# Optimization experiments

Measured on AMD Instinct MI355X. Metric: run time of the kernel, lower is better.

Reference implementation:

```python
import jax, jax.numpy as jnp
import numpy as np

N = 100000       # nodes
E = 3200000      # edges
F_IN = 128       # num_node_features
DIM = 32         # hidden dim (fixed in Net1)
L = 3            # num_layers
C = 10           # num_classes


def setup_inputs() -> dict:
    key = jax.random.key(0)
    ks = jax.random.split(key, 16)
    x = jax.random.normal(ks[0], (N, F_IN), dtype=jnp.float32)
    src = jax.random.randint(ks[1], (E,), 0, N, dtype=jnp.int32)
    dst = jax.random.randint(ks[2], (E,), 0, N, dtype=jnp.int32)
    def glorot(k, shape):
        lim = np.sqrt(6.0 / (shape[0] + shape[1])).astype(np.float32)
        return jax.random.uniform(k, shape, jnp.float32, -lim, lim)
    dims = [F_IN, DIM, DIM]
    inp = {"x": x, "src": src, "dst": dst}
    for i in range(L):
        din = dims[i]
        inp[f"Wn{i}"] = glorot(ks[3 + 3 * i], (din, DIM))      # neighbor weight
        inp[f"bn{i}"] = jnp.zeros((DIM,), jnp.float32)          # neighbor bias
        inp[f"Ws{i}"] = glorot(ks[4 + 3 * i], (din, DIM))      # self weight (no bias)
    inp["fc_w"] = glorot(ks[13], (DIM * L + F_IN, C))
    inp["fc_b"] = jnp.zeros((C,), jnp.float32)
    return inp


def _graph_conv_wl(x, src, dst, Wn, bn, Ws):
    # GraphConv(norm='none'): transform then aggregate (sum over in-neighbors)
    h = x @ Wn                                   # [N, DIM]
    msg = h[src]                                 # [E, DIM] gather
    agg = jax.ops.segment_sum(msg, dst, num_segments=N)  # [N, DIM] scatter-add
    return agg + bn + x @ Ws


def reference(x, src, dst, Wn0, bn0, Ws0, Wn1, bn1, Ws1, Wn2, bn2, Ws2, fc_w, fc_b):
    params = [(Wn0, bn0, Ws0), (Wn1, bn1, Ws1), (Wn2, bn2, Ws2)]
    xs = [x]
    h = x
    for Wn, bn, Ws in params:
        h = jax.nn.relu(_graph_conv_wl(h, src, dst, Wn, bn, Ws))
        xs.append(h)
    h = jnp.concatenate(xs, axis=1)              # [N, 128 + 3*32]
    logits = h @ fc_w + fc_b                     # [N, C]
    return jax.nn.log_softmax(logits, axis=1)
```

## Files before the change

kernel.cpp:

```cpp
#include <hip/hip_runtime.h>
#include <cstdint>

#define NN 100000
#define EE 3200000
#define SB_BITS 8
#define SB_NODES (1 << SB_BITS)
#define NSB ((NN + SB_NODES - 1) / SB_NODES)
#define CAP 9216
#define CH 4096
#define EPT (CH / 256)

__device__ inline float4 add4(float4 a, float4 b) {
    return make_float4(a.x + b.x, a.y + b.y, a.z + b.z, a.w + b.w);
}

__device__ inline unsigned pk_bf2(float lo, float hi) {
    unsigned a = __float_as_uint(lo);
    unsigned b = __float_as_uint(hi);
    a = (a + 0x7FFFu + ((a >> 16) & 1u)) >> 16;
    b = (b + 0x7FFFu + ((b >> 16) & 1u)) & 0xFFFF0000u;
    return a | b;
}


__global__ void k_hist_sb(const int* __restrict__ dst, int* __restrict__ scnt) {
    __shared__ int h[NSB];
    for (int i = threadIdx.x; i < NSB; i += 256) h[i] = 0;
    __syncthreads();
    for (int e = blockIdx.x * 256 + threadIdx.x; e < EE; e += gridDim.x * 256)
        atomicAdd(&h[dst[e] >> SB_BITS], 1);
    __syncthreads();
    for (int i = threadIdx.x; i < NSB; i += 256) {
        int v = h[i];
        if (v) atomicAdd(&scnt[i], v);
    }
}

__global__ void k_scan_sb(const int* __restrict__ scnt,
                          int* __restrict__ sbptr, int* __restrict__ cursor) {
    __shared__ int sm[512];
    int i = threadIdx.x;
    int v0 = (i < NSB) ? scnt[i] : 0;
    int v1 = (i + 256 < NSB) ? scnt[i + 256] : 0;
    sm[i] = v0;
    sm[i + 256] = v1;
    __syncthreads();
    for (int o = 1; o < 512; o <<= 1) {
        int a0 = (i >= o) ? sm[i - o] : 0;
        int a1 = (i + 256 >= o) ? sm[i + 256 - o] : 0;
        __syncthreads();
        sm[i] += a0;
        sm[i + 256] += a1;
        __syncthreads();
    }
    if (i < NSB)       { sbptr[i]       = sm[i] - v0;       cursor[i]       = sm[i] - v0; }
    if (i + 256 < NSB) { sbptr[i + 256] = sm[i + 256] - v1; cursor[i + 256] = sm[i + 256] - v1; }
    if (i == 0) sbptr[NSB] = sm[511];
}

__global__ void k_split(const int* __restrict__ src, const int* __restrict__ dst,
                        int* __restrict__ cursor, int* __restrict__ out) {
    __shared__ int hist[512];
    __shared__ int lbase[NSB];
    __shared__ int gbase[NSB];
    __shared__ int buf[CH];
    __shared__ unsigned short keyb[CH];
    const int nchunks = (EE + CH - 1) / CH;
    for (int c = blockIdx.x; c < nchunks; c += gridDim.x) {
        int base = c * CH;
        int cnt = min(CH, EE - base);
        hist[threadIdx.x] = 0;
        hist[threadIdx.x + 256] = 0;
        __syncthreads();
        int words[EPT], ranks[EPT], keys[EPT];
        #pragma unroll
        for (int k = 0; k < EPT; ++k) {
            int idx = threadIdx.x + k * 256;
            if (idx < cnt) {
                int d = dst[base + idx];
                int s = src[base + idx];
                int key = d >> SB_BITS;
                words[k] = s | ((d & (SB_NODES - 1)) << 17);
                keys[k] = key;
                ranks[k] = atomicAdd(&hist[key], 1);
            } else keys[k] = -1;
        }
        __syncthreads();
        int i = threadIdx.x;
        int v0 = hist[i], v1 = hist[i + 256];
        for (int o = 1; o < 512; o <<= 1) {
            int a0 = (i >= o) ? hist[i - o] : 0;
            int a1 = (i + 256 >= o) ? hist[i + 256 - o] : 0;
            __syncthreads();
            hist[i] += a0;
            hist[i + 256] += a1;
            __syncthreads();
        }
        if (i < NSB) {
            lbase[i] = hist[i] - v0;
            gbase[i] = (v0 > 0) ? atomicAdd(&cursor[i], v0) : 0;
        }
        if (i + 256 < NSB) {
            lbase[i + 256] = hist[i + 256] - v1;
            gbase[i + 256] = (v1 > 0) ? atomicAdd(&cursor[i + 256], v1) : 0;
        }
        __syncthreads();
        #pragma unroll
        for (int k = 0; k < EPT; ++k) {
            if (keys[k] >= 0) {
                int p = lbase[keys[k]] + ranks[k];
                buf[p] = words[k];
                keyb[p] = (unsigned short)keys[k];
            }
        }
        __syncthreads();
        for (int j = threadIdx.x; j < cnt; j += 256) {
            int kk = keyb[j];
            out[gbase[kk] + (j - lbase[kk])] = buf[j];
        }
        __syncthreads();
    }
}

__global__ void k_sb_sort(const int* __restrict__ sbptr, const int* __restrict__ packed,
                          int* __restrict__ csr_src, int* __restrict__ rowptr) {
    __shared__ int hist[SB_NODES];
    __shared__ int lbuf[CAP];
    int b = blockIdx.x;
    int e0 = sbptr[b], e1 = sbptr[b + 1];
    int cnt = e1 - e0;
    hist[threadIdx.x] = 0;
    __syncthreads();
    for (int j = e0 + threadIdx.x; j < e1; j += 256)
        atomicAdd(&hist[(packed[j] >> 17) & (SB_NODES - 1)], 1);
    __syncthreads();
    int i = threadIdx.x;
    int v = hist[i];
    for (int o = 1; o < 256; o <<= 1) {
        int a = (i >= o) ? hist[i - o] : 0;
        __syncthreads();
        hist[i] += a;
        __syncthreads();
    }
    int excl = hist[i] - v;
    int node = (b << SB_BITS) + i;
    if (node < NN) rowptr[node] = e0 + excl;
    hist[i] = excl;
    if (b == 0 && i == 0) rowptr[NN] = EE;
    __syncthreads();
    if (cnt <= CAP) {
        for (int j = e0 + threadIdx.x; j < e1; j += 256) {
            int w = packed[j];
            int n = (w >> 17) & (SB_NODES - 1);
            int pos = atomicAdd(&hist[n], 1);
            lbuf[pos] = w & 0x1FFFF;
        }
        __syncthreads();
        for (int j = threadIdx.x; j < cnt; j += 256)
            csr_src[e0 + j] = lbuf[j];
    } else {
        for (int j = e0 + threadIdx.x; j < e1; j += 256) {
            int w = packed[j];
            int n = (w >> 17) & (SB_NODES - 1);
            int pos = atomicAdd(&hist[n], 1);
            csr_src[e0 + pos] = w & 0x1FFFF;
        }
    }
}


template <int DIN>
__global__ __launch_bounds__(256) void k_transform(
        const float* __restrict__ h,
        const float* __restrict__ Wn,
        const float* __restrict__ Ws,
        const float* __restrict__ bn,
        unsigned* __restrict__ t_bf,
        float* __restrict__ hout) {
    constexpr int KC = 16;
    __shared__ float hs[256 * (KC + 1)];
    const int which = blockIdx.x & 1;
    const int node = (blockIdx.x >> 1) * 256 + threadIdx.x;
    const bool valid = node < NN;
    const float* __restrict__ W = which ? Ws : Wn;
    const float* __restrict__ hr = h + (size_t)(valid ? node : NN - 1) * DIN;
    float acc[32];
    #pragma unroll
    for (int d = 0; d < 32; ++d) acc[d] = 0.f;
    for (int kc = 0; kc < DIN; kc += KC) {
        __syncthreads();
        #pragma unroll
        for (int j = 0; j < KC / 4; ++j) {
            float4 f = *(const float4*)(hr + kc + j * 4);
            hs[threadIdx.x * (KC + 1) + j * 4 + 0] = f.x;
            hs[threadIdx.x * (KC + 1) + j * 4 + 1] = f.y;
            hs[threadIdx.x * (KC + 1) + j * 4 + 2] = f.z;
            hs[threadIdx.x * (KC + 1) + j * 4 + 3] = f.w;
        }
        __syncthreads();
        #pragma unroll
        for (int kk = 0; kk < KC; ++kk) {
            float f = hs[threadIdx.x * (KC + 1) + kk];
            const float* __restrict__ w0 = W + (kc + kk) * 32;
            #pragma unroll
            for (int d = 0; d < 32; ++d) acc[d] = fmaf(f, w0[d], acc[d]);
        }
    }
    if (valid) {
        if (which) {
            float* __restrict__ hp = hout + (size_t)node * 32;
            #pragma unroll
            for (int d = 0; d < 32; d += 4)
                *(float4*)(hp + d) = make_float4(acc[d] + bn[d], acc[d + 1] + bn[d + 1],
                                                 acc[d + 2] + bn[d + 2], acc[d + 3] + bn[d + 3]);
        } else {
            unsigned tb[16];
            #pragma unroll
            for (int d = 0; d < 16; ++d) tb[d] = pk_bf2(acc[2 * d], acc[2 * d + 1]);
            unsigned* tp = t_bf + (size_t)node * 16;
            #pragma unroll
            for (int d = 0; d < 16; d += 4)
                *(uint4*)(tp + d) = make_uint4(tb[d], tb[d + 1], tb[d + 2], tb[d + 3]);
        }
    }
}

__global__ void k_aggregate(const int* __restrict__ rowptr,
                            const int* __restrict__ csr_src,
                            const uint2* __restrict__ t2,
                            float4* __restrict__ hout4) {
    int node = blockIdx.x * 32 + (threadIdx.x >> 3);
    int q = threadIdx.x & 7;
    if (node >= NN) return;
    int j = rowptr[node];
    int end = rowptr[node + 1];
    float4 a0 = make_float4(0.f, 0.f, 0.f, 0.f);
    float4 a1 = a0, a2 = a0, a3 = a0;
    for (; j + 4 <= end; j += 4) {
        int s0 = csr_src[j];
        int s1 = csr_src[j + 1];
        int s2 = csr_src[j + 2];
        int s3 = csr_src[j + 3];
        uint2 u0 = t2[s0 * 8 + q];
        uint2 u1 = t2[s1 * 8 + q];
        uint2 u2 = t2[s2 * 8 + q];
        uint2 u3 = t2[s3 * 8 + q];
        a0.x += __uint_as_float(u0.x << 16); a0.y += __uint_as_float(u0.x & 0xFFFF0000u);
        a0.z += __uint_as_float(u0.y << 16); a0.w += __uint_as_float(u0.y & 0xFFFF0000u);
        a1.x += __uint_as_float(u1.x << 16); a1.y += __uint_as_float(u1.x & 0xFFFF0000u);
        a1.z += __uint_as_float(u1.y << 16); a1.w += __uint_as_float(u1.y & 0xFFFF0000u);
        a2.x += __uint_as_float(u2.x << 16); a2.y += __uint_as_float(u2.x & 0xFFFF0000u);
        a2.z += __uint_as_float(u2.y << 16); a2.w += __uint_as_float(u2.y & 0xFFFF0000u);
        a3.x += __uint_as_float(u3.x << 16); a3.y += __uint_as_float(u3.x & 0xFFFF0000u);
        a3.z += __uint_as_float(u3.y << 16); a3.w += __uint_as_float(u3.y & 0xFFFF0000u);
    }
    for (; j < end; ++j) {
        uint2 u = t2[csr_src[j] * 8 + q];
        a0.x += __uint_as_float(u.x << 16); a0.y += __uint_as_float(u.x & 0xFFFF0000u);
        a0.z += __uint_as_float(u.y << 16); a0.w += __uint_as_float(u.y & 0xFFFF0000u);
    }
    float4 s = add4(add4(a0, a1), add4(a2, a3));
    int idx = node * 8 + q;
    float4 h = hout4[idx];
    h.x = fmaxf(h.x + s.x, 0.f);
    h.y = fmaxf(h.y + s.y, 0.f);
    h.z = fmaxf(h.z + s.z, 0.f);
    h.w = fmaxf(h.w + s.w, 0.f);
    hout4[idx] = h;
}

__global__ void k_final(const float* __restrict__ x,
                        const float* __restrict__ h1,
                        const float* __restrict__ h2,
                        const float* __restrict__ h3,
                        const float* __restrict__ fc_w,
                        const float* __restrict__ fc_b,
                        float* __restrict__ out) {
    __shared__ float Wl[224 * 10];
    __shared__ float bl[10];
    for (int i = threadIdx.x; i < 224 * 10; i += blockDim.x) Wl[i] = fc_w[i];
    if (threadIdx.x < 10) bl[threadIdx.x] = fc_b[threadIdx.x];
    __syncthreads();
    int n = blockIdx.x * blockDim.x + threadIdx.x;
    if (n >= NN) return;
    float acc[10];
    #pragma unroll
    for (int c = 0; c < 10; ++c) acc[c] = bl[c];
    const float* xr = x + (size_t)n * 128;
    for (int j = 0; j < 128; ++j) {
        float f = xr[j];
        #pragma unroll
        for (int c = 0; c < 10; ++c) acc[c] += f * Wl[j * 10 + c];
    }
    const float* hs[3] = {h1, h2, h3};
    for (int l = 0; l < 3; ++l) {
        const float* hr = hs[l] + (size_t)n * 32;
        for (int j = 0; j < 32; ++j) {
            float f = hr[j];
            #pragma unroll
            for (int c = 0; c < 10; ++c) acc[c] += f * Wl[(128 + l * 32 + j) * 10 + c];
        }
    }
    float m = acc[0];
    #pragma unroll
    for (int c = 1; c < 10; ++c) m = fmaxf(m, acc[c]);
    float s = 0.f;
    #pragma unroll
    for (int c = 0; c < 10; ++c) s += __expf(acc[c] - m);
    float ls = __logf(s);
    #pragma unroll
    for (int c = 0; c < 10; ++c) out[n * 10 + c] = acc[c] - m - ls;
}

extern "C" void kernel_launch(void* const* d_in, const int* in_sizes, int n_in,
                              void* d_out, int out_size, void* d_ws, size_t ws_size,
                              hipStream_t stream) {
    const float* x   = (const float*)d_in[0];
    const int*   src = (const int*)d_in[1];
    const int*   dst = (const int*)d_in[2];
    const float* Wn[3] = {(const float*)d_in[3], (const float*)d_in[6], (const float*)d_in[9]};
    const float* bn[3] = {(const float*)d_in[4], (const float*)d_in[7], (const float*)d_in[10]};
    const float* Ws[3] = {(const float*)d_in[5], (const float*)d_in[8], (const float*)d_in[11]};
    const float* fc_w = (const float*)d_in[12];
    const float* fc_b = (const float*)d_in[13];
    float* out = (float*)d_out;

    char* w = (char*)d_ws;
    const size_t NF = (size_t)NN * 32;
    unsigned* t_bf = (unsigned*)w;              w += (size_t)NN * 16 * 4;
    float* h1  = (float*)w;                     w += NF * 4;
    float* h2  = (float*)w;                     w += NF * 4;
    float* h3  = (float*)w;                     w += NF * 4;
    int* csr_src = (int*)w;                     w += (size_t)EE * 4;
    int* scnt   = (int*)w;                      w += (size_t)NSB * 4;
    int* sbptr  = (int*)w;                      w += (size_t)(NSB + 1) * 4;
    int* cursor = (int*)w;                      w += (size_t)NSB * 4;
    int* rowptr = (int*)w;                      w += (size_t)(NN + 1) * 4;
    int* packed = (int*)h3;

    hipMemsetAsync(scnt, 0, (size_t)NSB * 4, stream);
    k_hist_sb<<<512, 256, 0, stream>>>(dst, scnt);
    k_scan_sb<<<1, 256, 0, stream>>>(scnt, sbptr, cursor);
    k_split<<<512, 256, 0, stream>>>(src, dst, cursor, packed);
    k_sb_sort<<<NSB, 256, 0, stream>>>(sbptr, packed, csr_src, rowptr);

    const int tr_blocks = 2 * ((NN + 255) / 256);
    const int ag_blocks = (NN + 31) / 32;
    k_transform<128><<<tr_blocks, 256, 0, stream>>>(x, Wn[0], Ws[0], bn[0], t_bf, h1);
    k_aggregate<<<ag_blocks, 256, 0, stream>>>(rowptr, csr_src, (const uint2*)t_bf, (float4*)h1);
    k_transform<32><<<tr_blocks, 256, 0, stream>>>(h1, Wn[1], Ws[1], bn[1], t_bf, h2);
    k_aggregate<<<ag_blocks, 256, 0, stream>>>(rowptr, csr_src, (const uint2*)t_bf, (float4*)h2);
    k_transform<32><<<tr_blocks, 256, 0, stream>>>(h2, Wn[2], Ws[2], bn[2], t_bf, h3);
    k_aggregate<<<ag_blocks, 256, 0, stream>>>(rowptr, csr_src, (const uint2*)t_bf, (float4*)h3);
    k_final<<<(NN + 255) / 256, 256, 0, stream>>>(x, h1, h2, h3, fc_w, fc_b, out);
}
```

Baseline: 452.5 us.

## Compute neighbor and self transforms in one thread, dropping LDS staging

```diff
diff --git a/kernel.cpp b/kernel.cpp
--- a/kernel.cpp
+++ b/kernel.cpp
@@ -170,59 +170,52 @@
 
 
 template <int DIN>
-__global__ __launch_bounds__(256) void k_transform(
+__global__ __launch_bounds__(64) void k_transform(
         const float* __restrict__ h,
         const float* __restrict__ Wn,
         const float* __restrict__ Ws,
         const float* __restrict__ bn,
         unsigned* __restrict__ t_bf,
         float* __restrict__ hout) {
-    constexpr int KC = 16;
-    __shared__ float hs[256 * (KC + 1)];
-    const int which = blockIdx.x & 1;
-    const int node = (blockIdx.x >> 1) * 256 + threadIdx.x;
-    const bool valid = node < NN;
-    const float* __restrict__ W = which ? Ws : Wn;
-    const float* __restrict__ hr = h + (size_t)(valid ? node : NN - 1) * DIN;
-    float acc[32];
-    #pragma unroll
-    for (int d = 0; d < 32; ++d) acc[d] = 0.f;
-    for (int kc = 0; kc < DIN; kc += KC) {
-        __syncthreads();
+    const int node = blockIdx.x * 64 + threadIdx.x;
+    if (node >= NN) return;
+    const float* __restrict__ hr = h + (size_t)node * DIN;
+    float accn[32], accs[32];
+    #pragma unroll
+    for (int d = 0; d < 32; ++d) { accn[d] = 0.f; accs[d] = 0.f; }
+    constexpr int NK4 = DIN / 4;
+    float4 f0 = *(const float4*)(hr);
+    float4 f1 = *(const float4*)(hr + 4);
+    #pragma unroll 4
+    for (int k4 = 0; k4 < NK4; ++k4) {
+        float4 cur = f0;
+        f0 = f1;
+        if (k4 + 2 < NK4) f1 = *(const float4*)(hr + (k4 + 2) * 4);
+        float fj[4] = {cur.x, cur.y, cur.z, cur.w};
         #pragma unroll
-        for (int j = 0; j < KC / 4; ++j) {
-            float4 f = *(const float4*)(hr + kc + j * 4);
-            hs[threadIdx.x * (KC + 1) + j * 4 + 0] = f.x;
-            hs[threadIdx.x * (KC + 1) + j * 4 + 1] = f.y;
-            hs[threadIdx.x * (KC + 1) + j * 4 + 2] = f.z;
-            hs[threadIdx.x * (KC + 1) + j * 4 + 3] = f.w;
-        }
-        __syncthreads();
-        #pragma unroll
-        for (int kk = 0; kk < KC; ++kk) {
-            float f = hs[threadIdx.x * (KC + 1) + kk];
-            const float* __restrict__ w0 = W + (kc + kk) * 32;
+        for (int j = 0; j < 4; ++j) {
+            float fv = fj[j];
+            const float* __restrict__ wn = Wn + (k4 * 4 + j) * 32;
+            const float* __restrict__ ws = Ws + (k4 * 4 + j) * 32;
             #pragma unroll
-            for (int d = 0; d < 32; ++d) acc[d] = fmaf(f, w0[d], acc[d]);
-        }
-    }
-    if (valid) {
-        if (which) {
-            float* __restrict__ hp = hout + (size_t)node * 32;
-            #pragma unroll
-            for (int d = 0; d < 32; d += 4)
-                *(float4*)(hp + d) = make_float4(acc[d] + bn[d], acc[d + 1] + bn[d + 1],
-                                                 acc[d + 2] + bn[d + 2], acc[d + 3] + bn[d + 3]);
-        } else {
-            unsigned tb[16];
-            #pragma unroll
-            for (int d = 0; d < 16; ++d) tb[d] = pk_bf2(acc[2 * d], acc[2 * d + 1]);
-            unsigned* tp = t_bf + (size_t)node * 16;
-            #pragma unroll
-            for (int d = 0; d < 16; d += 4)
-                *(uint4*)(tp + d) = make_uint4(tb[d], tb[d + 1], tb[d + 2], tb[d + 3]);
-        }
-    }
+            for (int d = 0; d < 32; ++d) {
+                accn[d] = fmaf(fv, wn[d], accn[d]);
+                accs[d] = fmaf(fv, ws[d], accs[d]);
+            }
+        }
+    }
+    unsigned tb[16];
+    #pragma unroll
+    for (int d = 0; d < 16; ++d) tb[d] = pk_bf2(accn[2 * d], accn[2 * d + 1]);
+    unsigned* tp = t_bf + (size_t)node * 16;
+    #pragma unroll
+    for (int d = 0; d < 16; d += 4)
+        *(uint4*)(tp + d) = make_uint4(tb[d], tb[d + 1], tb[d + 2], tb[d + 3]);
+    float* __restrict__ hp = hout + (size_t)node * 32;
+    #pragma unroll
+    for (int d = 0; d < 32; d += 4)
+        *(float4*)(hp + d) = make_float4(accs[d] + bn[d], accs[d + 1] + bn[d + 1],
+                                         accs[d + 2] + bn[d + 2], accs[d + 3] + bn[d + 3]);
 }
 
 __global__ void k_aggregate(const int* __restrict__ rowptr,
@@ -344,13 +337,13 @@
     k_split<<<512, 256, 0, stream>>>(src, dst, cursor, packed);
     k_sb_sort<<<NSB, 256, 0, stream>>>(sbptr, packed, csr_src, rowptr);
 
-    const int tr_blocks = 2 * ((NN + 255) / 256);
+    const int tr_blocks = (NN + 63) / 64;
     const int ag_blocks = (NN + 31) / 32;
-    k_transform<128><<<tr_blocks, 256, 0, stream>>>(x, Wn[0], Ws[0], bn[0], t_bf, h1);
+    k_transform<128><<<tr_blocks, 64, 0, stream>>>(x, Wn[0], Ws[0], bn[0], t_bf, h1);
     k_aggregate<<<ag_blocks, 256, 0, stream>>>(rowptr, csr_src, (const uint2*)t_bf, (float4*)h1);
-    k_transform<32><<<tr_blocks, 256, 0, stream>>>(h1, Wn[1], Ws[1], bn[1], t_bf, h2);
+    k_transform<32><<<tr_blocks, 64, 0, stream>>>(h1, Wn[1], Ws[1], bn[1], t_bf, h2);
     k_aggregate<<<ag_blocks, 256, 0, stream>>>(rowptr, csr_src, (const uint2*)t_bf, (float4*)h2);
-    k_transform<32><<<tr_blocks, 256, 0, stream>>>(h2, Wn[2], Ws[2], bn[2], t_bf, h3);
+    k_transform<32><<<tr_blocks, 64, 0, stream>>>(h2, Wn[2], Ws[2], bn[2], t_bf, h3);
     k_aggregate<<<ag_blocks, 256, 0, stream>>>(rowptr, csr_src, (const uint2*)t_bf, (float4*)h3);
     k_final<<<(NN + 255) / 256, 256, 0, stream>>>(x, h1, h2, h3, fc_w, fc_b, out);
 }
```

Result: slower. 612.3 us (+35.3%).

## Restructure node transform with LDS-staged weights and register tiling

Applied to the files above, without the earlier changes.

```diff
diff --git a/kernel.cpp b/kernel.cpp
--- a/kernel.cpp
+++ b/kernel.cpp
@@ -170,57 +170,83 @@
 
 
 template <int DIN>
-__global__ __launch_bounds__(256) void k_transform(
+__global__ __launch_bounds__(256, 3) void k_transform(
         const float* __restrict__ h,
         const float* __restrict__ Wn,
         const float* __restrict__ Ws,
         const float* __restrict__ bn,
         unsigned* __restrict__ t_bf,
         float* __restrict__ hout) {
-    constexpr int KC = 16;
-    __shared__ float hs[256 * (KC + 1)];
-    const int which = blockIdx.x & 1;
-    const int node = (blockIdx.x >> 1) * 256 + threadIdx.x;
-    const bool valid = node < NN;
-    const float* __restrict__ W = which ? Ws : Wn;
-    const float* __restrict__ hr = h + (size_t)(valid ? node : NN - 1) * DIN;
-    float acc[32];
-    #pragma unroll
-    for (int d = 0; d < 32; ++d) acc[d] = 0.f;
-    for (int kc = 0; kc < DIN; kc += KC) {
-        __syncthreads();
-        #pragma unroll
-        for (int j = 0; j < KC / 4; ++j) {
-            float4 f = *(const float4*)(hr + kc + j * 4);
-            hs[threadIdx.x * (KC + 1) + j * 4 + 0] = f.x;
-            hs[threadIdx.x * (KC + 1) + j * 4 + 1] = f.y;
-            hs[threadIdx.x * (KC + 1) + j * 4 + 2] = f.z;
-            hs[threadIdx.x * (KC + 1) + j * 4 + 3] = f.w;
-        }
-        __syncthreads();
-        #pragma unroll
-        for (int kk = 0; kk < KC; ++kk) {
-            float f = hs[threadIdx.x * (KC + 1) + kk];
-            const float* __restrict__ w0 = W + (kc + kk) * 32;
+    __shared__ float wlds[DIN * 64];
+    for (int i = threadIdx.x; i < DIN * 16; i += 256) {
+        int k = i >> 4, c = i & 15;
+        const float* sp = (c < 8) ? (Wn + k * 32 + c * 4) : (Ws + k * 32 + (c - 8) * 4);
+        *(float4*)(&wlds[k * 64 + c * 4]) = *(const float4*)sp;
+    }
+    __syncthreads();
+
+    const int lane = threadIdx.x & 63;
+    const int wv   = threadIdx.x >> 6;
+    const int q    = lane & 15;
+    const int slot = lane >> 4;
+    const int nbase = blockIdx.x * 128 + wv * 32 + slot * 8;
+    const float* __restrict__ wq = wlds + q * 4;
+
+    const float* xp[8];
+    #pragma unroll
+    for (int r = 0; r < 8; ++r) {
+        int n = nbase + r;
+        xp[r] = h + (size_t)(n < NN ? n : NN - 1) * DIN;
+    }
+
+    float acc0[8], acc1[8], acc2[8], acc3[8];
+    #pragma unroll
+    for (int r = 0; r < 8; ++r) { acc0[r] = 0.f; acc1[r] = 0.f; acc2[r] = 0.f; acc3[r] = 0.f; }
+
+    float4 xa[8], xb[8];
+
+    auto ldtile = [&](float4 (&dst)[8], int t) {
+        #pragma unroll
+        for (int r = 0; r < 8; ++r) dst[r] = *(const float4*)(xp[r] + t * 4);
+    };
+    auto comp4 = [&](const float4 (&xt)[8], int t) {
+        #pragma unroll
+        for (int kk = 0; kk < 4; ++kk) {
+            float4 w4 = *(const float4*)(wq + (t * 4 + kk) * 64);
             #pragma unroll
-            for (int d = 0; d < 32; ++d) acc[d] = fmaf(f, w0[d], acc[d]);
-        }
-    }
-    if (valid) {
-        if (which) {
-            float* __restrict__ hp = hout + (size_t)node * 32;
-            #pragma unroll
-            for (int d = 0; d < 32; d += 4)
-                *(float4*)(hp + d) = make_float4(acc[d] + bn[d], acc[d + 1] + bn[d + 1],
-                                                 acc[d + 2] + bn[d + 2], acc[d + 3] + bn[d + 3]);
+            for (int r = 0; r < 8; ++r) {
+                float xv = (kk == 0) ? xt[r].x : (kk == 1) ? xt[r].y
+                         : (kk == 2) ? xt[r].z : xt[r].w;
+                acc0[r] = fmaf(xv, w4.x, acc0[r]);
+                acc1[r] = fmaf(xv, w4.y, acc1[r]);
+                acc2[r] = fmaf(xv, w4.z, acc2[r]);
+                acc3[r] = fmaf(xv, w4.w, acc3[r]);
+            }
+        }
+    };
+
+    constexpr int T = DIN / 4;
+    ldtile(xa, 0);
+    for (int t = 0; t < T; t += 2) {
+        ldtile(xb, t + 1);
+        comp4(xa, t);
+        if (t + 2 < T) ldtile(xa, t + 2);
+        comp4(xb, t + 1);
+    }
+
+    float4 b4 = *(const float4*)(bn + (q >= 8 ? (q - 8) : 0) * 4);
+    #pragma unroll
+    for (int r = 0; r < 8; ++r) {
+        int node = nbase + r;
+        if (node >= NN) continue;
+        if (q < 8) {
+            unsigned w0 = pk_bf2(acc0[r], acc1[r]);
+            unsigned w1 = pk_bf2(acc2[r], acc3[r]);
+            *(uint2*)(t_bf + (size_t)node * 16 + q * 2) = make_uint2(w0, w1);
         } else {
-            unsigned tb[16];
-            #pragma unroll
-            for (int d = 0; d < 16; ++d) tb[d] = pk_bf2(acc[2 * d], acc[2 * d + 1]);
-            unsigned* tp = t_bf + (size_t)node * 16;
-            #pragma unroll
-            for (int d = 0; d < 16; d += 4)
-                *(uint4*)(tp + d) = make_uint4(tb[d], tb[d + 1], tb[d + 2], tb[d + 3]);
+            int ds = (q - 8) * 4;
+            *(float4*)(hout + (size_t)node * 32 + ds) =
+                make_float4(acc0[r] + b4.x, acc1[r] + b4.y, acc2[r] + b4.z, acc3[r] + b4.w);
         }
     }
 }
@@ -344,7 +370,7 @@
     k_split<<<512, 256, 0, stream>>>(src, dst, cursor, packed);
     k_sb_sort<<<NSB, 256, 0, stream>>>(sbptr, packed, csr_src, rowptr);
 
-    const int tr_blocks = 2 * ((NN + 255) / 256);
+    const int tr_blocks = (NN + 127) / 128;
     const int ag_blocks = (NN + 31) / 32;
     k_transform<128><<<tr_blocks, 256, 0, stream>>>(x, Wn[0], Ws[0], bn[0], t_bf, h1);
     k_aggregate<<<ag_blocks, 256, 0, stream>>>(rowptr, csr_src, (const uint2*)t_bf, (float4*)h1);
```

After: 728.6 us. +61.0%, slower.
